# Optimization experiments

Measured on AMD Instinct MI355X. Metric: run time of the kernel, lower is better.

Reference implementation:

```python
import jax, jax.numpy as jnp
import numpy as np

C = 1.0
SQC = C ** 0.5
EPS = 1e-15

def _artanh(x):
    return jnp.arctanh(jnp.clip(x, -1 + 1e-5, 1 - 1e-5))

def _norm(x):
    return jnp.sqrt(jnp.maximum(jnp.sum(x * x, -1, keepdims=True), EPS))

def expmap0(u):
    un = _norm(u)
    return jnp.tanh(SQC * un) * u / (SQC * un)

def logmap0(x):
    xn = _norm(x)
    return _artanh(SQC * xn) * x / (SQC * xn)

def project(x):
    maxnorm = (1.0 - 1e-3) / SQC
    xn = _norm(x)
    return jnp.where(xn > maxnorm, x / xn * maxnorm, x)

def mobius_add(x, y):
    x2 = jnp.sum(x * x, -1, keepdims=True)
    y2 = jnp.sum(y * y, -1, keepdims=True)
    xy = jnp.sum(x * y, -1, keepdims=True)
    num = (1 + 2 * C * xy + C * y2) * x + (1 - C * x2) * y
    den = 1 + 2 * C * xy + C * C * x2 * y2
    return num / jnp.maximum(den, EPS)

def mobius_matvec(M, x):
    xn = _norm(x)
    Mx = x @ M.T
    Mxn = _norm(Mx)
    res = jnp.tanh(Mxn / xn * _artanh(SQC * xn)) * Mx / (Mxn * SQC)
    return jnp.where(Mxn <= 1e-7, jnp.zeros_like(res), res)

def mobius_pointwise_mul(w, x):
    xn = _norm(x)
    wx = w * x
    wxn = _norm(wx)
    res = jnp.tanh(wxn / xn * _artanh(SQC * xn)) * wx / (wxn * SQC)
    return jnp.where(wxn <= 1e-7, jnp.zeros_like(res), res)

def mobius_scalar_mul(r, x):
    # r: [B,1] scalars, x: [P] point -> [B,P]
    xn = _norm(x)
    return jnp.tanh(r * _artanh(SQC * xn)) * x / (xn * SQC)

def poincare_dist(x, y):
    return 2.0 / SQC * _artanh(SQC * _norm(mobius_add(-x, y)))

def dist2plane(x, p, a):
    # x: [B,P], p,a: [K,P] -> [B,K]
    diff = mobius_add(-p[None, :, :], x[:, None, :])  # [B,K,P]
    diff2 = jnp.sum(diff * diff, -1)
    sc_da = jnp.sum(diff * a[None, :, :], -1)
    a_norm = jnp.sqrt(jnp.maximum(jnp.sum(a * a, -1), EPS))  # [K]
    num = 2 * SQC * sc_da
    den = jnp.maximum((1 - C * diff2) * a_norm[None, :], EPS)
    return jnp.arcsinh(num / den) / SQC

def one_rnn_transform(W, h, U, x, b):
    Wh = mobius_matvec(W, h)
    Ux = mobius_matvec(U, x)
    return mobius_add(mobius_add(Wh, Ux), b)

def mobius_gru(x_seq, w_ih, w_hh, b, h0):
    # x_seq: [S,B,E]; w_ih: [3,H,E]; w_hh: [3,H,H]; b: [3,H]
    W_ir, W_ih_, W_iz = w_ih[0], w_ih[1], w_ih[2]
    W_hr, W_hh_, W_hz = w_hh[0], w_hh[1], w_hh[2]
    b_r, b_h, b_z = b[0], b[1], b[2]

    def cell(h, x):
        z = jax.nn.sigmoid(logmap0(one_rnn_transform(W_hz, h, W_iz, x, b_z)))
        r = jax.nn.sigmoid(logmap0(one_rnn_transform(W_hr, h, W_ir, x, b_r)))
        rh = mobius_pointwise_mul(r, h)
        h_tilde = one_rnn_transform(W_hh_, rh, W_ih_, x, b_h)
        delta = mobius_add(-h, h_tilde)
        h_new = mobius_add(h, mobius_pointwise_mul(z, delta))
        return h_new, None

    h_final, _ = jax.lax.scan(cell, h0, x_seq)
    return h_final

def mobius_linear(x, W, b):
    return project(mobius_add(mobius_matvec(W, x), b))


def setup_inputs() -> dict:
    key = jax.random.key(0)
    ks = jax.random.split(key, 20)
    V, E, H, P, K, B, S = 32000, 256, 512, 256, 2, 512, 100
    inp = {
        "embedding": jax.random.normal(ks[0], (V, E), jnp.float32) * 0.1,
        "w_ih_src": jax.random.normal(ks[1], (3, H, E), jnp.float32) * 0.05,
        "w_hh_src": jax.random.normal(ks[2], (3, H, H), jnp.float32) * 0.05,
        "b_src": jax.random.normal(ks[3], (3, H), jnp.float32) * 0.01,
        "w_ih_tgt": jax.random.normal(ks[4], (3, H, E), jnp.float32) * 0.05,
        "w_hh_tgt": jax.random.normal(ks[5], (3, H, H), jnp.float32) * 0.05,
        "b_tgt": jax.random.normal(ks[6], (3, H), jnp.float32) * 0.01,
        "wp_src": jax.random.normal(ks[7], (P, H), jnp.float32) * 0.05,
        "bp_src": jax.random.normal(ks[8], (P,), jnp.float32) * 0.01,
        "wp_tgt": jax.random.normal(ks[9], (P, H), jnp.float32) * 0.05,
        "bp_tgt": jax.random.normal(ks[10], (P,), jnp.float32) * 0.01,
        "dist_bias": jax.random.normal(ks[11], (P,), jnp.float32) * 0.01,
        "plane_p": jax.random.normal(ks[12], (K, P), jnp.float32) * 0.01,
        "plane_a": jax.random.normal(ks[13], (K, P), jnp.float32) * 0.1,
        "source_tokens": jax.random.randint(ks[14], (B, S), 0, V, jnp.int32),
        "target_tokens": jax.random.randint(ks[15], (B, S), 0, V, jnp.int32),
        "alignment": jax.random.randint(ks[16], (B,), 0, B, jnp.int32),
    }
    return inp


def reference(embedding, w_ih_src, w_hh_src, b_src, w_ih_tgt, w_hh_tgt, b_tgt,
              wp_src, bp_src, wp_tgt, bp_tgt, dist_bias, plane_p, plane_a,
              source_tokens, target_tokens, alignment):
    B, S = source_tokens.shape
    H = w_hh_src.shape[-1]
    # euclidean embeddings lifted to the Poincare ball (embedding_type='eucl', hyp cell)
    src = expmap0(embedding[source_tokens]).transpose(1, 0, 2)  # [S,B,E]
    tgt = expmap0(embedding[target_tokens]).transpose(1, 0, 2)
    h0 = jnp.zeros((B, H), src.dtype)
    h_src = mobius_gru(src, w_ih_src, w_hh_src, b_src, h0)
    h_tgt = mobius_gru(tgt, w_ih_tgt, w_hh_tgt, b_tgt, h0)
    h_tgt = h_tgt[alignment]
    src_proj = mobius_linear(h_src, wp_src, bp_src)
    tgt_proj = mobius_linear(h_tgt, wp_tgt, bp_tgt)
    projected = mobius_add(src_proj, tgt_proj)
    d2 = poincare_dist(h_src, h_tgt) ** 2  # [B,1]
    bias = mobius_scalar_mul(d2, dist_bias)  # [B,P]
    projected = mobius_add(projected, bias)
    logits = dist2plane(projected, plane_p, plane_a)  # [B,K]
    return logits
```

## Files before the change

kernel.cpp:

```cpp
#include <hip/hip_runtime.h>
#include <hip/hip_bf16.h>

#define EPSF 1e-15f

typedef __hip_bfloat16 bf16;
typedef __attribute__((ext_vector_type(8))) short short8;
typedef __attribute__((ext_vector_type(4))) float f32x4;

#define F4E(v,i) ((i)==0?(v).x:((i)==1?(v).y:((i)==2?(v).z:(v).w)))
#define U4E(v,i) ((i)==0?(v).x:((i)==1?(v).y:((i)==2?(v).z:(v).w)))

__device__ __forceinline__ float artanh_c(float x) {
  x = fminf(fmaxf(x, -1.f + 1e-5f), 1.f - 1e-5f);
  return 0.5f * log1pf(2.f * x / (1.f - x));
}
__device__ __forceinline__ float sigmoidf(float x) { return 1.f / (1.f + expf(-x)); }
__device__ __forceinline__ float wave_sum(float x) {
#pragma unroll
  for (int o = 32; o > 0; o >>= 1) x += __shfl_xor(x, o);
  return x;
}
__device__ __forceinline__ float bu2f(ushort u) { return __uint_as_float(((unsigned)u) << 16); }
__device__ __forceinline__ ushort f2bu(float v) {
  bf16 t = __float2bfloat16(v);
  union { bf16 b; ushort u; } c; c.b = t; return c.u;
}
__device__ __forceinline__ void split2(float v, ushort& h, ushort& l) {
  h = f2bu(v); l = f2bu(v - bu2f(h));
}

__global__ __launch_bounds__(256) void k_wconv(
    const float* __restrict__ w_ih_src, const float* __restrict__ w_hh_src,
    const float* __restrict__ w_ih_tgt, const float* __restrict__ w_hh_tgt,
    bf16* __restrict__ W0h, bf16* __restrict__ W1h)
{
  const int idx = blockIdx.x * 256 + threadIdx.x;
  float v;
  if (idx < 1835008) {
    const int g = idx / 917504, p = idx % 917504;
    const float* wih = g ? w_ih_tgt : w_ih_src;
    const float* whh = g ? w_hh_tgt : w_hh_src;
    if (p < 524288) {
      const int unit = p >> 9, r = p & 511, lane = r >> 3, e = r & 7;
      const int ct = unit >> 4, ki = unit & 15;
      const int col = ct*16 + (lane & 15), k = ki*32 + (lane >> 4)*8 + e;
      v = (col < 512) ? whh[524288 + col*512 + k]
                      : whh[(col - 512)*512 + k];
    } else {
      const int q = p - 524288;
      const int unit = q >> 9, r = q & 511, lane = r >> 3, e = r & 7;
      const int ct = unit >> 3, ki = unit & 7;
      const int col = ct*16 + (lane & 15), k = ki*32 + (lane >> 4)*8 + e;
      v = (col < 512)  ? wih[262144 + col*256 + k]
        : (col < 1024) ? wih[(col - 512)*256 + k]
                       : wih[131072 + (col - 1024)*256 + k];
    }
    ((ushort*)W0h)[idx] = f2bu(v);
  } else {
    const int j = idx - 1835008;
    if (j >= 524288) return;
    const int g = j >> 18, p = j & 262143;
    const float* whh = g ? w_hh_tgt : w_hh_src;
    const int unit = p >> 9, r = p & 511, lane = r >> 3, e = r & 7;
    const int ct = unit >> 4, ki = unit & 15;
    const int col = ct*16 + (lane & 15), k = ki*32 + (lane >> 4)*8 + e;
    v = whh[262144 + col*512 + k];
    ((ushort*)W1h)[j] = f2bu(v);
  }
}

__device__ __forceinline__ void gate_row(
    const float h[8], const float whz[8], const float whr[8],
    const float uxz[8], const float uxr[8], const float uxh[8],
    const float bz[8], const float br[8],
    float xn_x, float axn_x,
    float rh[8], float pz[8], float puhx[8],
    float& o_xnrh, float& o_axnrh, float& o_y2u, float& o_sh2)
{
  float r60=0, r61=0, r62=0, r63=0, r64_=0, r65=0;
#pragma unroll
  for (int e = 0; e < 8; e++) {
    r60 += h[e]*h[e];     r61 += whz[e]*whz[e]; r62 += whr[e]*whr[e];
    r63 += uxz[e]*uxz[e]; r64_ += uxr[e]*uxr[e]; r65 += uxh[e]*uxh[e];
  }
  r60 = wave_sum(r60); r61 = wave_sum(r61); r62 = wave_sum(r62);
  r63 = wave_sum(r63); r64_ = wave_sum(r64_); r65 = wave_sum(r65);
  const float sh2 = r60;
  const float xn_h = sqrtf(fmaxf(sh2, EPSF)), axn_h = artanh_c(xn_h);
  const float mz = sqrtf(fmaxf(r61, EPSF)); const float tz = tanhf(mz / xn_h * axn_h);
  const float sz = (mz <= 1e-7f) ? 0.f : tz/mz; const float x2z = (mz <= 1e-7f) ? 0.f : tz*tz;
  const float mr = sqrtf(fmaxf(r62, EPSF)); const float tr_ = tanhf(mr / xn_h * axn_h);
  const float sr = (mr <= 1e-7f) ? 0.f : tr_/mr; const float x2r = (mr <= 1e-7f) ? 0.f : tr_*tr_;
  const float muz = sqrtf(fmaxf(r63, EPSF)); const float tuz = tanhf(muz / xn_x * axn_x);
  const float suz = (muz <= 1e-7f) ? 0.f : tuz/muz; const float y2z = (muz <= 1e-7f) ? 0.f : tuz*tuz;
  const float mur = sqrtf(fmaxf(r64_, EPSF)); const float tur = tanhf(mur / xn_x * axn_x);
  const float sur = (mur <= 1e-7f) ? 0.f : tur/mur; const float y2r = (mur <= 1e-7f) ? 0.f : tur*tur;
  const float muh = sqrtf(fmaxf(r65, EPSF)); const float tuh = tanhf(muh / xn_x * axn_x);
  const float suh = (muh <= 1e-7f) ? 0.f : tuh/muh; const float y2u = (muh <= 1e-7f) ? 0.f : tuh*tuh;

  float dd0 = 0, dd1 = 0;
#pragma unroll
  for (int e = 0; e < 8; e++) {
    dd0 += (sz*whz[e])*(suz*uxz[e]);
    dd1 += (sr*whr[e])*(sur*uxr[e]);
  }
  dd0 = wave_sum(dd0); dd1 = wave_sum(dd1);
  float t1z[8], t1r[8];
  {
    const float iv = 1.f / fmaxf(1.f + 2.f*dd0 + x2z*y2z, EPSF);
    const float c1 = 1.f + 2.f*dd0 + y2z, c2 = 1.f - x2z;
#pragma unroll
    for (int e = 0; e < 8; e++) t1z[e] = (c1*(sz*whz[e]) + c2*(suz*uxz[e])) * iv;
  }
  {
    const float iv = 1.f / fmaxf(1.f + 2.f*dd1 + x2r*y2r, EPSF);
    const float c1 = 1.f + 2.f*dd1 + y2r, c2 = 1.f - x2r;
#pragma unroll
    for (int e = 0; e < 8; e++) t1r[e] = (c1*(sr*whr[e]) + c2*(sur*uxr[e])) * iv;
  }
  float e0=0, e1=0, e2=0, e3=0, e4=0, e5=0;
#pragma unroll
  for (int e = 0; e < 8; e++) {
    e0 += t1z[e]*t1z[e]; e1 += t1z[e]*bz[e]; e2 += bz[e]*bz[e];
    e3 += t1r[e]*t1r[e]; e4 += t1r[e]*br[e]; e5 += br[e]*br[e];
  }
  e0 = wave_sum(e0); e1 = wave_sum(e1); e2 = wave_sum(e2);
  e3 = wave_sum(e3); e4 = wave_sum(e4); e5 = wave_sum(e5);
  float t2z[8], t2r[8];
  {
    const float iv = 1.f / fmaxf(1.f + 2.f*e1 + e0*e2, EPSF);
    const float c1 = 1.f + 2.f*e1 + e2, c2 = 1.f - e0;
#pragma unroll
    for (int e = 0; e < 8; e++) t2z[e] = (c1*t1z[e] + c2*bz[e]) * iv;
  }
  {
    const float iv = 1.f / fmaxf(1.f + 2.f*e4 + e3*e5, EPSF);
    const float c1 = 1.f + 2.f*e4 + e5, c2 = 1.f - e3;
#pragma unroll
    for (int e = 0; e < 8; e++) t2r[e] = (c1*t1r[e] + c2*br[e]) * iv;
  }
  float n0 = 0, n1 = 0;
#pragma unroll
  for (int e = 0; e < 8; e++) { n0 += t2z[e]*t2z[e]; n1 += t2r[e]*t2r[e]; }
  n0 = wave_sum(n0); n1 = wave_sum(n1);
  const float nz = sqrtf(fmaxf(n0, EPSF)); const float fz = artanh_c(nz) / nz;
  const float nr = sqrtf(fmaxf(n1, EPSF)); const float frg = artanh_c(nr) / nr;
  float wx[8];
  float rw = 0;
#pragma unroll
  for (int e = 0; e < 8; e++) {
    pz[e] = sigmoidf(fz * t2z[e]);
    const float rr = sigmoidf(frg * t2r[e]);
    wx[e] = rr * h[e];
    rw += wx[e]*wx[e];
  }
  rw = wave_sum(rw);
  const float wxn = sqrtf(fmaxf(rw, EPSF));
  const float trh = tanhf(wxn / xn_h * axn_h);
  const float srh = (wxn <= 1e-7f) ? 0.f : trh / wxn;
  const float xn_rh = (wxn <= 1e-7f) ? sqrtf(EPSF) : fmaxf(trh, sqrtf(EPSF));
#pragma unroll
  for (int e = 0; e < 8; e++) { rh[e] = srh * wx[e]; puhx[e] = suh * uxh[e]; }
  o_xnrh = xn_rh; o_axnrh = artanh_c(xn_rh); o_y2u = y2u; o_sh2 = sh2;
}

__device__ __forceinline__ void update_row(
    const float mt_[8], const float bh[8],
    const float pz[8], const float puhx[8], const float phv[8],
    float p_xnrh, float p_axnrh, float p_y2u, float p_sh2,
    float hnew[8])
{
  float a0s = 0, a1s = 0;
#pragma unroll
  for (int e = 0; e < 8; e++) { a0s += mt_[e]*mt_[e]; a1s += mt_[e]*puhx[e]; }
  a0s = wave_sum(a0s); a1s = wave_sum(a1s);
  const float m = sqrtf(fmaxf(a0s, EPSF));
  const float tt = tanhf(m / p_xnrh * p_axnrh);
  const float st = (m <= 1e-7f) ? 0.f : tt/m;
  const float x2 = (m <= 1e-7f) ? 0.f : tt*tt;
  float t1[8];
  {
    const float xy = st * a1s;
    const float iv = 1.f / fmaxf(1.f + 2.f*xy + x2*p_y2u, EPSF);
    const float c1 = 1.f + 2.f*xy + p_y2u, c2 = 1.f - x2;
#pragma unroll
    for (int e = 0; e < 8; e++) t1[e] = (c1*(st*mt_[e]) + c2*puhx[e]) * iv;
  }
  float b0s = 0, b1s = 0, b2s = 0;
#pragma unroll
  for (int e = 0; e < 8; e++) { b0s += t1[e]*t1[e]; b1s += t1[e]*bh[e]; b2s += bh[e]*bh[e]; }
  b0s = wave_sum(b0s); b1s = wave_sum(b1s); b2s = wave_sum(b2s);
  float ht[8];
  {
    const float iv = 1.f / fmaxf(1.f + 2.f*b1s + b0s*b2s, EPSF);
    const float c1 = 1.f + 2.f*b1s + b2s, c2 = 1.f - b0s;
#pragma unroll
    for (int e = 0; e < 8; e++) ht[e] = (c1*t1[e] + c2*bh[e]) * iv;
  }
  float c0s = 0, c1s = 0;
#pragma unroll
  for (int e = 0; e < 8; e++) { c0s += ht[e]*ht[e]; c1s += phv[e]*ht[e]; }
  c0s = wave_sum(c0s); c1s = wave_sum(c1s);
  float delta[8];
  {
    const float xy = -c1s;
    const float iv = 1.f / fmaxf(1.f + 2.f*xy + p_sh2*c0s, EPSF);
    const float c1 = 1.f + 2.f*xy + c0s, c2 = 1.f - p_sh2;
#pragma unroll
    for (int e = 0; e < 8; e++) delta[e] = (c1*(-phv[e]) + c2*ht[e]) * iv;
  }
  float d0s = 0, d1s = 0, d2s = 0;
#pragma unroll
  for (int e = 0; e < 8; e++) {
    const float ww = pz[e]*delta[e];
    d0s += delta[e]*delta[e]; d1s += ww*ww; d2s += phv[e]*ww;
  }
  d0s = wave_sum(d0s); d1s = wave_sum(d1s); d2s = wave_sum(d2s);
  const float dn = sqrtf(fmaxf(d0s, EPSF));
  const float axnd = artanh_c(dn);
  const float wxn = sqrtf(fmaxf(d1s, EPSF));
  const float tzd = tanhf(wxn / dn * axnd);
  const float szd = (wxn <= 1e-7f) ? 0.f : tzd/wxn;
  const float y2zd = (wxn <= 1e-7f) ? 0.f : tzd*tzd;
  const float xy = szd * d2s;
  const float iv = 1.f / fmaxf(1.f + 2.f*xy + p_sh2*y2zd, EPSF);
  const float c1 = 1.f + 2.f*xy + y2zd, c2 = 1.f - p_sh2;
#pragma unroll
  for (int e = 0; e < 8; e++) hnew[e] = (c1*phv[e] + c2*(szd*pz[e]*delta[e])) * iv;
}

__global__ __launch_bounds__(512, 1) void k_rnn(
    const float* __restrict__ emb, const int* __restrict__ src_t,
    const int* __restrict__ tgt_t, const float* __restrict__ b_src,
    const float* __restrict__ b_tgt,
    const bf16* __restrict__ W0h_, const bf16* __restrict__ W1h_,
    float* __restrict__ yws, float* __restrict__ htmws,
    float* __restrict__ hbuf)
{
  const int bid = blockIdx.x, tid = threadIdx.x;
  const int w = tid >> 6, lane = tid & 63;
  const int fr = lane & 15, kg = lane >> 4;
  const int xcd = bid & 7, slot = bid >> 3;
  const int g = xcd >> 2;
  const int b16 = (xcd & 3) * 8 + slot;
  const bf16* W0h = W0h_ + (size_t)g * 917504;
  const bf16* W1h = W1h_ + (size_t)g * 262144;
  const int* toks = g ? tgt_t : src_t;
  const float* bb = g ? b_tgt : b_src;
  float* ysl = yws + (size_t)bid * 40960;
  float* hsl = htmws + (size_t)bid * 8192;

  __shared__ char L[65536];
  for (int i = tid; i < 2048; i += 512) ((float4*)L)[i] = make_float4(0.f,0.f,0.f,0.f);

  float p_xnx[2], p_axnx[2];
  float pz_[2][8], puhx_[2][8], phh_[2][8];
  float p_xnrh[2], p_axnrh[2], p_y2u[2], p_sh2[2];

#define XLOAD(RI, TOKIDX)                                                        \
  {                                                                              \
    const int row = w*2 + (RI);                                                  \
    const int tok = toks[(b16*16 + row)*100 + (TOKIDX)];                         \
    const float4 ev = ((const float4*)(emb + (size_t)tok * 256))[lane];          \
    float ss = ev.x*ev.x + ev.y*ev.y + ev.z*ev.z + ev.w*ev.w;                    \
    ss = wave_sum(ss);                                                           \
    const float un = sqrtf(fmaxf(ss, EPSF));                                     \
    const float fac = tanhf(un) / un;                                            \
    const float xnv = sqrtf(fmaxf(fac*fac*ss, EPSF));                            \
    p_xnx[RI] = xnv; p_axnx[RI] = artanh_c(xnv);                                 \
    ushort th[4], tl[4];                                                         \
    split2(fac*ev.x, th[0], tl[0]); split2(fac*ev.y, th[1], tl[1]);              \
    split2(fac*ev.z, th[2], tl[2]); split2(fac*ev.w, th[3], tl[3]);              \
    const unsigned xo = (unsigned)((row*512 + lane*8) ^ ((row & 7) << 4));       \
    *(ushort4*)(L + 32768 + xo) = make_ushort4(th[0],th[1],th[2],th[3]);         \
    *(ushort4*)(L + 40960 + xo) = make_ushort4(tl[0],tl[1],tl[2],tl[3]);         \
  }

  XLOAD(0, 0)
  XLOAD(1, 0)
  __syncthreads();

  for (int s = 0; s < 100; s++) {
    {
      const f32x4 z4 = {0.f,0.f,0.f,0.f};
      f32x4 acc[8];
#pragma unroll
      for (int t = 0; t < 8; t++) acc[t] = z4;
#pragma unroll 2
      for (int ki = 0; ki < 16; ki++) {
        short8 bfr[8];
#pragma unroll
        for (int t = 0; t < 8; t++)
          bfr[t] = *(const short8*)(W0h + (size_t)(((w*8 + t)*16 + ki)*512) + lane*8);
        const unsigned ao = (unsigned)((fr*1024 + ki*64 + kg*16) ^ ((fr & 7) << 4));
        const short8 aHi = *(const short8*)(L + ao);
        const short8 aLo = *(const short8*)(L + 16384 + ao);
#pragma unroll
        for (int t = 0; t < 8; t++) {
          acc[t] = __builtin_amdgcn_mfma_f32_16x16x32_bf16(aHi, bfr[t], acc[t], 0,0,0);
          acc[t] = __builtin_amdgcn_mfma_f32_16x16x32_bf16(aLo, bfr[t], acc[t], 0,0,0);
        }
      }
#pragma unroll
      for (int t = 0; t < 8; t++) {
        const int colb = (w*8 + t)*16 + fr;
#pragma unroll
        for (int r = 0; r < 4; r++)
          ysl[(size_t)(kg*4 + r)*2560 + colb] = acc[t][r];
      }
    }
    {
      const f32x4 z4 = {0.f,0.f,0.f,0.f};
      f32x4 acc[12];
#pragma unroll
      for (int t = 0; t < 12; t++) acc[t] = z4;
      for (int ki = 0; ki < 8; ki++) {
        short8 bfr[12];
#pragma unroll
        for (int t = 0; t < 12; t++)
          bfr[t] = *(const short8*)(W0h + 524288 + (size_t)(((w*12 + t)*8 + ki)*512) + lane*8);
        const unsigned ao = (unsigned)((fr*512 + ki*64 + kg*16) ^ ((fr & 7) << 4));
        const short8 aHi = *(const short8*)(L + 32768 + ao);
        const short8 aLo = *(const short8*)(L + 40960 + ao);
#pragma unroll
        for (int t = 0; t < 12; t++) {
          acc[t] = __builtin_amdgcn_mfma_f32_16x16x32_bf16(aHi, bfr[t], acc[t], 0,0,0);
          acc[t] = __builtin_amdgcn_mfma_f32_16x16x32_bf16(aLo, bfr[t], acc[t], 0,0,0);
        }
      }
#pragma unroll
      for (int t = 0; t < 12; t++) {
        const int colb = 1024 + (w*12 + t)*16 + fr;
#pragma unroll
        for (int r = 0; r < 4; r++)
          ysl[(size_t)(kg*4 + r)*2560 + colb] = acc[t][r];
      }
    }
    __syncthreads();

#define PH2_ROW(RI)                                                              \
    {                                                                            \
      const int row = w*2 + (RI);                                                \
      const float* grow = ysl + row * 2560;                                      \
      float h[8], whz[8], whr[8], uxz[8], uxr[8], uxh[8], bz[8], br[8];          \
      _Pragma("unroll")                                                          \
      for (int q = 0; q < 2; q++) {                                              \
        const int j4 = lane + 64*q;                                              \
        const unsigned ho = (unsigned)((row*1024 + j4*8) ^ ((row & 7) << 4));    \
        const ushort4 hh4 = *(const ushort4*)(L + ho);                           \
        const ushort4 hl4 = *(const ushort4*)(L + 16384 + ho);                   \
        const float4 vz  = ((const float4*)grow)[j4];                            \
        const float4 vr  = ((const float4*)(grow + 512))[j4];                    \
        const float4 uz  = ((const float4*)(grow + 1024))[j4];                   \
        const float4 ur  = ((const float4*)(grow + 1536))[j4];                   \
        const float4 uh  = ((const float4*)(grow + 2048))[j4];                   \
        const float4 vbz = ((const float4*)(bb + 1024))[j4];                     \
        const float4 vbr = ((const float4*)bb)[j4];                              \
        _Pragma("unroll")                                                        \
        for (int i = 0; i < 4; i++) {                                            \
          const int e = q*4 + i;                                                 \
          h[e] = bu2f(U4E(hh4,i)) + bu2f(U4E(hl4,i));                            \
          whz[e] = F4E(vz,i); whr[e] = F4E(vr,i);                                \
          uxz[e] = F4E(uz,i); uxr[e] = F4E(ur,i); uxh[e] = F4E(uh,i);            \
          bz[e] = F4E(vbz,i); br[e] = F4E(vbr,i);                               \
        }                                                                        \
      }                                                                          \
      float rh[8];                                                               \
      gate_row(h, whz, whr, uxz, uxr, uxh, bz, br, p_xnx[RI], p_axnx[RI],        \
               rh, pz_[RI], puhx_[RI],                                           \
               p_xnrh[RI], p_axnrh[RI], p_y2u[RI], p_sh2[RI]);                   \
      _Pragma("unroll")                                                          \
      for (int e = 0; e < 8; e++) phh_[RI][e] = h[e];                            \
      _Pragma("unroll")                                                          \
      for (int q = 0; q < 2; q++) {                                              \
        const int j4 = lane + 64*q;                                              \
        const unsigned ro = (unsigned)((row*1024 + j4*8) ^ ((row & 7) << 4));    \
        ushort th[4], tl[4];                                                     \
        _Pragma("unroll")                                                        \
        for (int i = 0; i < 4; i++) split2(rh[q*4+i], th[i], tl[i]);             \
        *(ushort4*)(L + 32768 + ro) = make_ushort4(th[0],th[1],th[2],th[3]);     \
        *(ushort4*)(L + 49152 + ro) = make_ushort4(tl[0],tl[1],tl[2],tl[3]);     \
      }                                                                          \
    }

    PH2_ROW(0)
    PH2_ROW(1)
    __syncthreads();

    {
      const f32x4 z4 = {0.f,0.f,0.f,0.f};
      f32x4 acc[4];
#pragma unroll
      for (int t = 0; t < 4; t++) acc[t] = z4;
#pragma unroll 2
      for (int ki = 0; ki < 16; ki++) {
        short8 bfr[4];
#pragma unroll
        for (int t = 0; t < 4; t++)
          bfr[t] = *(const short8*)(W1h + (size_t)(((w*4 + t)*16 + ki)*512) + lane*8);
        const unsigned ao = (unsigned)((fr*1024 + ki*64 + kg*16) ^ ((fr & 7) << 4));
        const short8 aHi = *(const short8*)(L + 32768 + ao);
        const short8 aLo = *(const short8*)(L + 49152 + ao);
#pragma unroll
        for (int t = 0; t < 4; t++) {
          acc[t] = __builtin_amdgcn_mfma_f32_16x16x32_bf16(aHi, bfr[t], acc[t], 0,0,0);
          acc[t] = __builtin_amdgcn_mfma_f32_16x16x32_bf16(aLo, bfr[t], acc[t], 0,0,0);
        }
      }
#pragma unroll
      for (int t = 0; t < 4; t++) {
        const int colb = (w*4 + t)*16 + fr;
#pragma unroll
        for (int r = 0; r < 4; r++)
          hsl[(size_t)(kg*4 + r)*512 + colb] = acc[t][r];
      }
    }
    __syncthreads();

#define PH4_ROW(RI)                                                              \
    {                                                                            \
      const int row = w*2 + (RI);                                                \
      float mt_[8], bh[8];                                                       \
      _Pragma("unroll")                                                          \
      for (int q = 0; q < 2; q++) {                                              \
        const int j4 = lane + 64*q;                                              \
        const float4 vm = ((const float4*)(hsl + row*512))[j4];                  \
        const float4 vb = ((const float4*)(bb + 512))[j4];                       \
        _Pragma("unroll")                                                        \
        for (int i = 0; i < 4; i++) {                                            \
          mt_[q*4+i] = F4E(vm,i); bh[q*4+i] = F4E(vb,i);                         \
        }                                                                        \
      }                                                                          \
      float hnew[8];                                                             \
      update_row(mt_, bh, pz_[RI], puhx_[RI], phh_[RI],                          \
                 p_xnrh[RI], p_axnrh[RI], p_y2u[RI], p_sh2[RI], hnew);           \
      _Pragma("unroll")                                                          \
      for (int q = 0; q < 2; q++) {                                              \
        const int j4 = lane + 64*q;                                              \
        const unsigned ho = (unsigned)((row*1024 + j4*8) ^ ((row & 7) << 4));    \
        ushort th[4], tl[4];                                                     \
        _Pragma("unroll")                                                        \
        for (int i = 0; i < 4; i++) split2(hnew[q*4+i], th[i], tl[i]);           \
        *(ushort4*)(L + ho) = make_ushort4(th[0],th[1],th[2],th[3]);             \
        *(ushort4*)(L + 16384 + ho) = make_ushort4(tl[0],tl[1],tl[2],tl[3]);     \
        if (s == 99)                                                             \
          ((float4*)(hbuf + (size_t)(g*512 + b16*16 + row)*512))[j4] =           \
              make_float4(hnew[q*4], hnew[q*4+1], hnew[q*4+2], hnew[q*4+3]);     \
      }                                                                          \
      if (s + 1 < 100) XLOAD(RI, s + 1)                                          \
    }

    PH4_ROW(0)
    PH4_ROW(1)
    __syncthreads();
  }
}

__global__ __launch_bounds__(256) void gemm_k(
    const float* __restrict__ hbuf,
    const float* __restrict__ wp_src, const float* __restrict__ wp_tgt,
    const int* __restrict__ alignment,
    float* __restrict__ out)
{
  const int rt = blockIdx.x, ct = blockIdx.y;
  const int rowBase = rt * 64;
  const int tid = threadIdx.x;
  const int chunk = ct >> 2;
  const int colBase = ct * 64, ldo = 512, kdim = 512;
  const float* W = (chunk ? wp_tgt : wp_src) + (size_t)((ct & 3) * 64) * 512;
  const int ar = tid >> 2, ak = (tid & 3) * 4;
  int arow = rowBase + ar;
  if (chunk) arow = 512 + alignment[arow];
  const float* Arow = hbuf + (size_t)arow * kdim;
  const float* Wrow = W + (size_t)(tid >> 2) * kdim + (tid & 3) * 4;

  __shared__ __align__(16) float As[16][68];
  __shared__ __align__(16) float Bs[16][68];
  float acc[4][4] = {{0.f}};
  const int ty = tid >> 4, tx = tid & 15;

  for (int k0 = 0; k0 < kdim; k0 += 16) {
    const float4 av = *(const float4*)(Arow + k0 + ak);
    const float4 bv = *(const float4*)(Wrow + k0);
    const int bj = tid >> 2;
    As[ak + 0][ar] = av.x; As[ak + 1][ar] = av.y; As[ak + 2][ar] = av.z; As[ak + 3][ar] = av.w;
    Bs[ak + 0][bj] = bv.x; Bs[ak + 1][bj] = bv.y; Bs[ak + 2][bj] = bv.z; Bs[ak + 3][bj] = bv.w;
    __syncthreads();
#pragma unroll
    for (int kk = 0; kk < 16; kk++) {
      const float4 a4 = *(const float4*)(&As[kk][ty * 4]);
      const float4 b4 = *(const float4*)(&Bs[kk][tx * 4]);
      acc[0][0] += a4.x * b4.x; acc[0][1] += a4.x * b4.y; acc[0][2] += a4.x * b4.z; acc[0][3] += a4.x * b4.w;
      acc[1][0] += a4.y * b4.x; acc[1][1] += a4.y * b4.y; acc[1][2] += a4.y * b4.z; acc[1][3] += a4.y * b4.w;
      acc[2][0] += a4.z * b4.x; acc[2][1] += a4.z * b4.y; acc[2][2] += a4.z * b4.z; acc[2][3] += a4.z * b4.w;
      acc[3][0] += a4.w * b4.x; acc[3][1] += a4.w * b4.y; acc[3][2] += a4.w * b4.z; acc[3][3] += a4.w * b4.w;
    }
    __syncthreads();
  }
#pragma unroll
  for (int r = 0; r < 4; r++) {
    float4 o; o.x = acc[r][0]; o.y = acc[r][1]; o.z = acc[r][2]; o.w = acc[r][3];
    *(float4*)(out + (size_t)(rowBase + ty * 4 + r) * ldo + colBase + tx * 4) = o;
  }
}

template<int N>
__device__ __forceinline__ void block_reduce(float* v) {
  __shared__ float s[4][N];
  __syncthreads();
  const int lane = threadIdx.x & 63;
  const int wv = threadIdx.x >> 6;
#pragma unroll
  for (int n = 0; n < N; n++) {
    float x = v[n];
#pragma unroll
    for (int o = 32; o > 0; o >>= 1) x += __shfl_down(x, o);
    if (lane == 0) s[wv][n] = x;
  }
  __syncthreads();
#pragma unroll
  for (int n = 0; n < N; n++) v[n] = s[0][n] + s[1][n] + s[2][n] + s[3][n];
}

__global__ __launch_bounds__(256) void k_head(
    const float* __restrict__ hb, const float* __restrict__ mxb,
    const float* __restrict__ bp_src, const float* __restrict__ bp_tgt,
    const float* __restrict__ dist_bias, const float* __restrict__ plane_p,
    const float* __restrict__ plane_a, const int* __restrict__ alignment,
    float* __restrict__ outp)
{
  const int b = blockIdx.x;
  const int t = threadIdx.x;
  const int arow = 512 + alignment[b];
  float hs[2], htg[2];
  hs[0] = hb[(size_t)b * 512 + t];      hs[1] = hb[(size_t)b * 512 + 256 + t];
  htg[0] = hb[(size_t)arow * 512 + t];  htg[1] = hb[(size_t)arow * 512 + 256 + t];
  const float mxs = mxb[(size_t)b * 512 + t];
  const float mxt = mxb[(size_t)b * 512 + 256 + t];
  const float bps = bp_src[t], bpt = bp_tgt[t], db = dist_bias[t];
  const float pp0 = plane_p[t], pp1 = plane_p[256 + t];
  const float pa0 = plane_a[t], pa1 = plane_a[256 + t];

  float rA[5] = {0, 0, 0, 0, 0};
#pragma unroll
  for (int e = 0; e < 2; e++) {
    rA[0] += hs[e] * hs[e]; rA[1] += htg[e] * htg[e]; rA[2] += hs[e] * htg[e];
  }
  rA[3] = mxs * mxs; rA[4] = mxt * mxt;
  block_reduce<5>(rA);
  const float shs = rA[0], sht = rA[1], dot_st = rA[2];
  const float xns = sqrtf(fmaxf(shs, EPSF)), axns = artanh_c(xns);
  const float xnt = sqrtf(fmaxf(sht, EPSF)), axnt = artanh_c(xnt);
  const float ms = sqrtf(fmaxf(rA[3], EPSF)); const float ts = tanhf(ms / xns * axns);
  const float ss = (ms <= 1e-7f) ? 0.f : ts / ms; const float x2s = (ms <= 1e-7f) ? 0.f : ts * ts;
  const float mt = sqrtf(fmaxf(rA[4], EPSF)); const float tt = tanhf(mt / xnt * axnt);
  const float st = (mt <= 1e-7f) ? 0.f : tt / mt; const float x2t = (mt <= 1e-7f) ? 0.f : tt * tt;
  const float vs = ss * mxs, vt = st * mxt;

  float rB[5] = {bps * bps, vs * bps, bpt * bpt, vt * bpt, db * db};
  block_reduce<5>(rB);
  float ps, pt;
  {
    const float y2 = rB[0], xy = rB[1];
    const float iv = 1.f / fmaxf(1.f + 2.f * xy + x2s * y2, EPSF);
    ps = ((1.f + 2.f * xy + y2) * vs + (1.f - x2s) * bps) * iv;
  }
  {
    const float y2 = rB[2], xy = rB[3];
    const float iv = 1.f / fmaxf(1.f + 2.f * xy + x2t * y2, EPSF);
    pt = ((1.f + 2.f * xy + y2) * vt + (1.f - x2t) * bpt) * iv;
  }
  float rC[2] = {ps * ps, pt * pt};
  block_reduce<2>(rC);
  {
    const float n = sqrtf(fmaxf(rC[0], EPSF));
    if (n > 0.999f) ps *= 0.999f / n;
  }
  {
    const float n = sqrtf(fmaxf(rC[1], EPSF));
    if (n > 0.999f) pt *= 0.999f / n;
  }
  float df[2];
  {
    const float xy = -dot_st;
    const float iv = 1.f / fmaxf(1.f + 2.f * xy + shs * sht, EPSF);
    const float c1 = 1.f + 2.f * xy + sht, c2 = 1.f - shs;
#pragma unroll
    for (int e = 0; e < 2; e++) df[e] = (c1 * (-hs[e]) + c2 * htg[e]) * iv;
  }
  float rD[4] = {ps * ps, pt * pt, ps * pt, df[0] * df[0] + df[1] * df[1]};
  block_reduce<4>(rD);
  float pr;
  {
    const float x2 = rD[0], y2 = rD[1], xy = rD[2];
    const float iv = 1.f / fmaxf(1.f + 2.f * xy + x2 * y2, EPSF);
    pr = ((1.f + 2.f * xy + y2) * ps + (1.f - x2) * pt) * iv;
  }
  const float dn = sqrtf(fmaxf(rD[3], EPSF));
  const float dist = 2.f * artanh_c(dn);
  const float d2v = dist * dist;
  const float dbn = sqrtf(fmaxf(rB[4], EPSF));
  const float biasv = tanhf(d2v * artanh_c(dbn)) * db / dbn;

  float rE[3] = {pr * pr, biasv * biasv, pr * biasv};
  block_reduce<3>(rE);
  float pr2;
  {
    const float x2 = rE[0], y2 = rE[1], xy = rE[2];
    const float iv = 1.f / fmaxf(1.f + 2.f * xy + x2 * y2, EPSF);
    pr2 = ((1.f + 2.f * xy + y2) * pr + (1.f - x2) * biasv) * iv;
  }
  float rF[5] = {pp0 * pp0, pp0 * pr2, pp1 * pp1, pp1 * pr2, pr2 * pr2};
  block_reduce<5>(rF);
  float d0, d1;
  {
    const float x2 = rF[0], xy = -rF[1], y2 = rF[4];
    const float iv = 1.f / fmaxf(1.f + 2.f * xy + x2 * y2, EPSF);
    d0 = ((1.f + 2.f * xy + y2) * (-pp0) + (1.f - x2) * pr2) * iv;
  }
  {
    const float x2 = rF[2], xy = -rF[3], y2 = rF[4];
    const float iv = 1.f / fmaxf(1.f + 2.f * xy + x2 * y2, EPSF);
    d1 = ((1.f + 2.f * xy + y2) * (-pp1) + (1.f - x2) * pr2) * iv;
  }
  float rG[6] = {d0 * d0, d0 * pa0, pa0 * pa0, d1 * d1, d1 * pa1, pa1 * pa1};
  block_reduce<6>(rG);
  if (t == 0) {
    const float an0 = sqrtf(fmaxf(rG[2], EPSF));
    const float an1 = sqrtf(fmaxf(rG[5], EPSF));
    outp[b * 2 + 0] = asinhf(2.f * rG[1] / fmaxf((1.f - rG[0]) * an0, EPSF));
    outp[b * 2 + 1] = asinhf(2.f * rG[4] / fmaxf((1.f - rG[3]) * an1, EPSF));
  }
}

extern "C" void kernel_launch(void* const* d_in, const int* in_sizes, int n_in,
                              void* d_out, int out_size, void* d_ws, size_t ws_size,
                              hipStream_t stream) {
  const float* emb       = (const float*)d_in[0];
  const float* w_ih_src  = (const float*)d_in[1];
  const float* w_hh_src  = (const float*)d_in[2];
  const float* b_src     = (const float*)d_in[3];
  const float* w_ih_tgt  = (const float*)d_in[4];
  const float* w_hh_tgt  = (const float*)d_in[5];
  const float* b_tgt     = (const float*)d_in[6];
  const float* wp_src    = (const float*)d_in[7];
  const float* bp_src    = (const float*)d_in[8];
  const float* wp_tgt    = (const float*)d_in[9];
  const float* bp_tgt    = (const float*)d_in[10];
  const float* dist_bias = (const float*)d_in[11];
  const float* plane_p   = (const float*)d_in[12];
  const float* plane_a   = (const float*)d_in[13];
  const int* src_t       = (const int*)d_in[14];
  const int* tgt_t       = (const int*)d_in[15];
  const int* alignment   = (const int*)d_in[16];
  float* outp            = (float*)d_out;

  char* wsb = (char*)d_ws;
  float* yws   = (float*)(wsb + 0);
  float* htmws = (float*)(wsb + 10485760);
  float* hbuf  = (float*)(wsb + 12582912);
  float* mxb   = (float*)(wsb + 14680064);
  bf16*  W0h   = (bf16*)(wsb + 15728640);
  bf16*  W1h   = (bf16*)(wsb + 19398656);

  k_wconv<<<9216, 256, 0, stream>>>(w_ih_src, w_hh_src, w_ih_tgt, w_hh_tgt,
                                    W0h, W1h);
  k_rnn<<<64, 512, 0, stream>>>(emb, src_t, tgt_t, b_src, b_tgt,
                                W0h, W1h, yws, htmws, hbuf);
  gemm_k<<<dim3(8, 8), 256, 0, stream>>>(hbuf, wp_src, wp_tgt, alignment, mxb);
  k_head<<<512, 256, 0, stream>>>(hbuf, mxb, bp_src, bp_tgt, dist_bias,
                                  plane_p, plane_a, alignment, outp);
}
```

Before: 8.191 ms.

## Split RNN batch across 128 blocks of 8 rows, store gates as bf16

The recurrent kernel now launches 128 blocks of 256 threads, each owning 8 batch rows instead of 16, so each wave computes twice as many output columns per MFMA pass. Only half of each 16-row MFMA tile is used, since rows 8-15 repeat rows 0-7. The gate pre-activation scratch is stored as bf16 in global memory, and the hidden-transform scratch moves from global memory into LDS. This spreads the serial 100-step recurrence over more CUs and halves scratch traffic. The cost is wasted MFMA work on the padded rows, twice the total weight streaming across blocks, and reduced precision in the stored gate values.

```diff
diff --git a/kernel.cpp b/kernel.cpp
--- a/kernel.cpp
+++ b/kernel.cpp
@@ -229,29 +229,28 @@
   for (int e = 0; e < 8; e++) hnew[e] = (c1*phv[e] + c2*(szd*pz[e]*delta[e])) * iv;
 }
 
-__global__ __launch_bounds__(512, 1) void k_rnn(
+__global__ __launch_bounds__(256, 1) void k_rnn(
     const float* __restrict__ emb, const int* __restrict__ src_t,
     const int* __restrict__ tgt_t, const float* __restrict__ b_src,
     const float* __restrict__ b_tgt,
     const bf16* __restrict__ W0h_, const bf16* __restrict__ W1h_,
-    float* __restrict__ yws, float* __restrict__ htmws,
-    float* __restrict__ hbuf)
+    ushort* __restrict__ yws, float* __restrict__ hbuf)
 {
   const int bid = blockIdx.x, tid = threadIdx.x;
   const int w = tid >> 6, lane = tid & 63;
   const int fr = lane & 15, kg = lane >> 4;
-  const int xcd = bid & 7, slot = bid >> 3;
-  const int g = xcd >> 2;
-  const int b16 = (xcd & 3) * 8 + slot;
+  const int fr7 = fr & 7;
+  const int g = (bid & 7) >> 2;
+  const int b8 = (bid & 3) * 16 + (bid >> 3);
   const bf16* W0h = W0h_ + (size_t)g * 917504;
   const bf16* W1h = W1h_ + (size_t)g * 262144;
   const int* toks = g ? tgt_t : src_t;
   const float* bb = g ? b_tgt : b_src;
-  float* ysl = yws + (size_t)bid * 40960;
-  float* hsl = htmws + (size_t)bid * 8192;
-
-  __shared__ char L[65536];
-  for (int i = tid; i < 2048; i += 512) ((float4*)L)[i] = make_float4(0.f,0.f,0.f,0.f);
+  ushort* yg = yws + (size_t)bid * 20480;
+
+  __shared__ char L[57600];
+  float* htmL = (float*)(L + 40960);
+  for (int i = tid; i < 1024; i += 256) ((float4*)L)[i] = make_float4(0.f,0.f,0.f,0.f);
 
   float p_xnx[2], p_axnx[2];
   float pz_[2][8], puhx_[2][8], phh_[2][8];
@@ -260,7 +259,7 @@
 #define XLOAD(RI, TOKIDX)                                                        \
   {                                                                              \
     const int row = w*2 + (RI);                                                  \
-    const int tok = toks[(b16*16 + row)*100 + (TOKIDX)];                         \
+    const int tok = toks[(b8*8 + row)*100 + (TOKIDX)];                           \
     const float4 ev = ((const float4*)(emb + (size_t)tok * 256))[lane];          \
     float ss = ev.x*ev.x + ev.y*ev.y + ev.z*ev.z + ev.w*ev.w;                    \
     ss = wave_sum(ss);                                                           \
@@ -272,8 +271,8 @@
     split2(fac*ev.x, th[0], tl[0]); split2(fac*ev.y, th[1], tl[1]);              \
     split2(fac*ev.z, th[2], tl[2]); split2(fac*ev.w, th[3], tl[3]);              \
     const unsigned xo = (unsigned)((row*512 + lane*8) ^ ((row & 7) << 4));       \
-    *(ushort4*)(L + 32768 + xo) = make_ushort4(th[0],th[1],th[2],th[3]);         \
-    *(ushort4*)(L + 40960 + xo) = make_ushort4(tl[0],tl[1],tl[2],tl[3]);         \
+    *(ushort4*)(L + 16384 + xo) = make_ushort4(th[0],th[1],th[2],th[3]);         \
+    *(ushort4*)(L + 20480 + xo) = make_ushort4(tl[0],tl[1],tl[2],tl[3]);         \
   }
 
   XLOAD(0, 0)
@@ -283,33 +282,35 @@
   for (int s = 0; s < 100; s++) {
     {
       const f32x4 z4 = {0.f,0.f,0.f,0.f};
-      f32x4 acc[8];
-#pragma unroll
-      for (int t = 0; t < 8; t++) acc[t] = z4;
-#pragma unroll 2
+      f32x4 acc[16];
+#pragma unroll
+      for (int t = 0; t < 16; t++) acc[t] = z4;
       for (int ki = 0; ki < 16; ki++) {
-        short8 bfr[8];
-#pragma unroll
-        for (int t = 0; t < 8; t++)
-          bfr[t] = *(const short8*)(W0h + (size_t)(((w*8 + t)*16 + ki)*512) + lane*8);
-        const unsigned ao = (unsigned)((fr*1024 + ki*64 + kg*16) ^ ((fr & 7) << 4));
+        short8 bfr[16];
+#pragma unroll
+        for (int t = 0; t < 16; t++)
+          bfr[t] = *(const short8*)(W0h + (size_t)(((w*16 + t)*16 + ki)*512) + lane*8);
+        const unsigned ao = (unsigned)((fr7*1024 + ki*64 + kg*16) ^ (fr7 << 4));
         const short8 aHi = *(const short8*)(L + ao);
-        const short8 aLo = *(const short8*)(L + 16384 + ao);
-#pragma unroll
-        for (int t = 0; t < 8; t++) {
+        const short8 aLo = *(const short8*)(L + 8192 + ao);
+#pragma unroll
+        for (int t = 0; t < 16; t++) {
           acc[t] = __builtin_amdgcn_mfma_f32_16x16x32_bf16(aHi, bfr[t], acc[t], 0,0,0);
           acc[t] = __builtin_amdgcn_mfma_f32_16x16x32_bf16(aLo, bfr[t], acc[t], 0,0,0);
         }
       }
-#pragma unroll
-      for (int t = 0; t < 8; t++) {
-        const int colb = (w*8 + t)*16 + fr;
-#pragma unroll
-        for (int r = 0; r < 4; r++)
-          ysl[(size_t)(kg*4 + r)*2560 + colb] = acc[t][r];
+      if (kg < 2) {
+#pragma unroll
+        for (int t = 0; t < 16; t++) {
+          const int colb = (w*16 + t)*16 + fr;
+#pragma unroll
+          for (int r = 0; r < 4; r++)
+            yg[(size_t)(kg*4 + r)*2560 + colb] = f2bu(acc[t][r]);
+        }
       }
     }
-    {
+#pragma unroll
+    for (int p = 0; p < 2; p++) {
       const f32x4 z4 = {0.f,0.f,0.f,0.f};
       f32x4 acc[12];
 #pragma unroll
@@ -318,22 +319,25 @@
         short8 bfr[12];
 #pragma unroll
         for (int t = 0; t < 12; t++)
-          bfr[t] = *(const short8*)(W0h + 524288 + (size_t)(((w*12 + t)*8 + ki)*512) + lane*8);
-        const unsigned ao = (unsigned)((fr*512 + ki*64 + kg*16) ^ ((fr & 7) << 4));
-        const short8 aHi = *(const short8*)(L + 32768 + ao);
-        const short8 aLo = *(const short8*)(L + 40960 + ao);
+          bfr[t] = *(const short8*)(W0h + 524288 +
+                      (size_t)(((w*24 + p*12 + t)*8 + ki)*512) + lane*8);
+        const unsigned ao = (unsigned)((fr7*512 + ki*64 + kg*16) ^ (fr7 << 4));
+        const short8 aHi = *(const short8*)(L + 16384 + ao);
+        const short8 aLo = *(const short8*)(L + 20480 + ao);
 #pragma unroll
         for (int t = 0; t < 12; t++) {
           acc[t] = __builtin_amdgcn_mfma_f32_16x16x32_bf16(aHi, bfr[t], acc[t], 0,0,0);
           acc[t] = __builtin_amdgcn_mfma_f32_16x16x32_bf16(aLo, bfr[t], acc[t], 0,0,0);
         }
       }
-#pragma unroll
-      for (int t = 0; t < 12; t++) {
-        const int colb = 1024 + (w*12 + t)*16 + fr;
-#pragma unroll
-        for (int r = 0; r < 4; r++)
-          ysl[(size_t)(kg*4 + r)*2560 + colb] = acc[t][r];
+      if (kg < 2) {
+#pragma unroll
+        for (int t = 0; t < 12; t++) {
+          const int colb = 1024 + (w*24 + p*12 + t)*16 + fr;
+#pragma unroll
+          for (int r = 0; r < 4; r++)
+            yg[(size_t)(kg*4 + r)*2560 + colb] = f2bu(acc[t][r]);
+        }
       }
     }
     __syncthreads();
@@ -341,27 +345,28 @@
 #define PH2_ROW(RI)                                                              \
     {                                                                            \
       const int row = w*2 + (RI);                                                \
-      const float* grow = ysl + row * 2560;                                      \
+      const ushort* growu = yg + (size_t)row * 2560;                             \
       float h[8], whz[8], whr[8], uxz[8], uxr[8], uxh[8], bz[8], br[8];          \
       _Pragma("unroll")                                                          \
       for (int q = 0; q < 2; q++) {                                              \
         const int j4 = lane + 64*q;                                              \
         const unsigned ho = (unsigned)((row*1024 + j4*8) ^ ((row & 7) << 4));    \
         const ushort4 hh4 = *(const ushort4*)(L + ho);                           \
-        const ushort4 hl4 = *(const ushort4*)(L + 16384 + ho);                   \
-        const float4 vz  = ((const float4*)grow)[j4];                            \
-        const float4 vr  = ((const float4*)(grow + 512))[j4];                    \
-        const float4 uz  = ((const float4*)(grow + 1024))[j4];                   \
-        const float4 ur  = ((const float4*)(grow + 1536))[j4];                   \
-        const float4 uh  = ((const float4*)(grow + 2048))[j4];                   \
+        const ushort4 hl4 = *(const ushort4*)(L + 8192 + ho);                    \
+        const ushort4 vz  = ((const ushort4*)growu)[j4];                         \
+        const ushort4 vr  = ((const ushort4*)(growu + 512))[j4];                 \
+        const ushort4 uz  = ((const ushort4*)(growu + 1024))[j4];                \
+        const ushort4 ur  = ((const ushort4*)(growu + 1536))[j4];                \
+        const ushort4 uh  = ((const ushort4*)(growu + 2048))[j4];                \
         const float4 vbz = ((const float4*)(bb + 1024))[j4];                     \
         const float4 vbr = ((const float4*)bb)[j4];                              \
         _Pragma("unroll")                                                        \
         for (int i = 0; i < 4; i++) {                                            \
           const int e = q*4 + i;                                                 \
           h[e] = bu2f(U4E(hh4,i)) + bu2f(U4E(hl4,i));                            \
-          whz[e] = F4E(vz,i); whr[e] = F4E(vr,i);                                \
-          uxz[e] = F4E(uz,i); uxr[e] = F4E(ur,i); uxh[e] = F4E(uh,i);            \
+          whz[e] = bu2f(U4E(vz,i)); whr[e] = bu2f(U4E(vr,i));                    \
+          uxz[e] = bu2f(U4E(uz,i)); uxr[e] = bu2f(U4E(ur,i));                    \
+          uxh[e] = bu2f(U4E(uh,i));                                              \
           bz[e] = F4E(vbz,i); br[e] = F4E(vbr,i);                               \
         }                                                                        \
       }                                                                          \
@@ -378,8 +383,8 @@
         ushort th[4], tl[4];                                                     \
         _Pragma("unroll")                                                        \
         for (int i = 0; i < 4; i++) split2(rh[q*4+i], th[i], tl[i]);             \
-        *(ushort4*)(L + 32768 + ro) = make_ushort4(th[0],th[1],th[2],th[3]);     \
-        *(ushort4*)(L + 49152 + ro) = make_ushort4(tl[0],tl[1],tl[2],tl[3]);     \
+        *(ushort4*)(L + 24576 + ro) = make_ushort4(th[0],th[1],th[2],th[3]);     \
+        *(ushort4*)(L + 32768 + ro) = make_ushort4(tl[0],tl[1],tl[2],tl[3]);     \
       }                                                                          \
     }
 
@@ -389,30 +394,31 @@
 
     {
       const f32x4 z4 = {0.f,0.f,0.f,0.f};
-      f32x4 acc[4];
-#pragma unroll
-      for (int t = 0; t < 4; t++) acc[t] = z4;
-#pragma unroll 2
+      f32x4 acc[8];
+#pragma unroll
+      for (int t = 0; t < 8; t++) acc[t] = z4;
       for (int ki = 0; ki < 16; ki++) {
-        short8 bfr[4];
-#pragma unroll
-        for (int t = 0; t < 4; t++)
-          bfr[t] = *(const short8*)(W1h + (size_t)(((w*4 + t)*16 + ki)*512) + lane*8);
-        const unsigned ao = (unsigned)((fr*1024 + ki*64 + kg*16) ^ ((fr & 7) << 4));
-        const short8 aHi = *(const short8*)(L + 32768 + ao);
-        const short8 aLo = *(const short8*)(L + 49152 + ao);
-#pragma unroll
-        for (int t = 0; t < 4; t++) {
+        short8 bfr[8];
+#pragma unroll
+        for (int t = 0; t < 8; t++)
+          bfr[t] = *(const short8*)(W1h + (size_t)(((w*8 + t)*16 + ki)*512) + lane*8);
+        const unsigned ao = (unsigned)((fr7*1024 + ki*64 + kg*16) ^ (fr7 << 4));
+        const short8 aHi = *(const short8*)(L + 24576 + ao);
+        const short8 aLo = *(const short8*)(L + 32768 + ao);
+#pragma unroll
+        for (int t = 0; t < 8; t++) {
           acc[t] = __builtin_amdgcn_mfma_f32_16x16x32_bf16(aHi, bfr[t], acc[t], 0,0,0);
           acc[t] = __builtin_amdgcn_mfma_f32_16x16x32_bf16(aLo, bfr[t], acc[t], 0,0,0);
         }
       }
-#pragma unroll
-      for (int t = 0; t < 4; t++) {
-        const int colb = (w*4 + t)*16 + fr;
-#pragma unroll
-        for (int r = 0; r < 4; r++)
-          hsl[(size_t)(kg*4 + r)*512 + colb] = acc[t][r];
+      if (kg < 2) {
+#pragma unroll
+        for (int t = 0; t < 8; t++) {
+          const int colb = (w*8 + t)*16 + fr;
+#pragma unroll
+          for (int r = 0; r < 4; r++)
+            htmL[(kg*4 + r)*520 + colb] = acc[t][r];
+        }
       }
     }
     __syncthreads();
@@ -424,7 +430,7 @@
       _Pragma("unroll")                                                          \
       for (int q = 0; q < 2; q++) {                                              \
         const int j4 = lane + 64*q;                                              \
-        const float4 vm = ((const float4*)(hsl + row*512))[j4];                  \
+        const float4 vm = ((const float4*)(htmL + row*520))[j4];                 \
         const float4 vb = ((const float4*)(bb + 512))[j4];                       \
         _Pragma("unroll")                                                        \
         for (int i = 0; i < 4; i++) {                                            \
@@ -442,9 +448,9 @@
         _Pragma("unroll")                                                        \
         for (int i = 0; i < 4; i++) split2(hnew[q*4+i], th[i], tl[i]);           \
         *(ushort4*)(L + ho) = make_ushort4(th[0],th[1],th[2],th[3]);             \
-        *(ushort4*)(L + 16384 + ho) = make_ushort4(tl[0],tl[1],tl[2],tl[3]);     \
+        *(ushort4*)(L + 8192 + ho) = make_ushort4(tl[0],tl[1],tl[2],tl[3]);      \
         if (s == 99)                                                             \
-          ((float4*)(hbuf + (size_t)(g*512 + b16*16 + row)*512))[j4] =           \
+          ((float4*)(hbuf + (size_t)(g*512 + b8*8 + row)*512))[j4] =             \
               make_float4(hnew[q*4], hnew[q*4+1], hnew[q*4+2], hnew[q*4+3]);     \
       }                                                                          \
       if (s + 1 < 100) XLOAD(RI, s + 1)                                          \
@@ -656,17 +662,16 @@
   float* outp            = (float*)d_out;
 
   char* wsb = (char*)d_ws;
-  float* yws   = (float*)(wsb + 0);
-  float* htmws = (float*)(wsb + 10485760);
-  float* hbuf  = (float*)(wsb + 12582912);
-  float* mxb   = (float*)(wsb + 14680064);
-  bf16*  W0h   = (bf16*)(wsb + 15728640);
-  bf16*  W1h   = (bf16*)(wsb + 19398656);
+  ushort* yws  = (ushort*)(wsb + 0);
+  float* hbuf  = (float*)(wsb + 5242880);
+  float* mxb   = (float*)(wsb + 7340032);
+  bf16*  W0h   = (bf16*)(wsb + 8388608);
+  bf16*  W1h   = (bf16*)(wsb + 12058624);
 
   k_wconv<<<9216, 256, 0, stream>>>(w_ih_src, w_hh_src, w_ih_tgt, w_hh_tgt,
                                     W0h, W1h);
-  k_rnn<<<64, 512, 0, stream>>>(emb, src_t, tgt_t, b_src, b_tgt,
-                                W0h, W1h, yws, htmws, hbuf);
+  k_rnn<<<128, 256, 0, stream>>>(emb, src_t, tgt_t, b_src, b_tgt,
+                                 W0h, W1h, yws, hbuf);
   gemm_k<<<dim3(8, 8), 256, 0, stream>>>(hbuf, wp_src, wp_tgt, alignment, mxb);
   k_head<<<512, 256, 0, stream>>>(hbuf, mxb, bp_src, bp_tgt, dist_bias,
                                   plane_p, plane_a, alignment, outp);
```

Measured after the change: 9.828 ms. +20.0%, slower.

## Keep GRU gate pre-activations in LDS as bf16 instead of global workspace

Applied to the files above, without the earlier changes.

The per-step gate GEMM outputs (16 rows x 2560 cols) are now written as bf16 into a swizzled region of enlarged dynamic shared memory (144KB) rather than as fp32 to a per-block global workspace slice. The pointwise phase reads them back from LDS. This removes a global write/read round trip on the sequential critical path of each of the 100 timesteps. In exchange the gate pre-activations lose precision to bf16, and LDS usage rises sharply. The unroll-2 pragmas on the MFMA k-loops are also dropped.

```diff
diff --git a/kernel.cpp b/kernel.cpp
--- a/kernel.cpp
+++ b/kernel.cpp
@@ -229,14 +229,15 @@
   for (int e = 0; e < 8; e++) hnew[e] = (c1*phv[e] + c2*(szd*pz[e]*delta[e])) * iv;
 }
 
+#define YADDR(row, byteoff) (65536u + ((unsigned)((row)*5120 + (byteoff)) ^ (((row)&7)<<4)))
 __global__ __launch_bounds__(512, 1) void k_rnn(
     const float* __restrict__ emb, const int* __restrict__ src_t,
     const int* __restrict__ tgt_t, const float* __restrict__ b_src,
     const float* __restrict__ b_tgt,
     const bf16* __restrict__ W0h_, const bf16* __restrict__ W1h_,
-    float* __restrict__ yws, float* __restrict__ htmws,
-    float* __restrict__ hbuf)
+    float* __restrict__ htmws, float* __restrict__ hbuf)
 {
+  extern __shared__ char L[];
   const int bid = blockIdx.x, tid = threadIdx.x;
   const int w = tid >> 6, lane = tid & 63;
   const int fr = lane & 15, kg = lane >> 4;
@@ -247,10 +248,8 @@
   const bf16* W1h = W1h_ + (size_t)g * 262144;
   const int* toks = g ? tgt_t : src_t;
   const float* bb = g ? b_tgt : b_src;
-  float* ysl = yws + (size_t)bid * 40960;
   float* hsl = htmws + (size_t)bid * 8192;
 
-  __shared__ char L[65536];
   for (int i = tid; i < 2048; i += 512) ((float4*)L)[i] = make_float4(0.f,0.f,0.f,0.f);
 
   float p_xnx[2], p_axnx[2];
@@ -286,7 +285,6 @@
       f32x4 acc[8];
 #pragma unroll
       for (int t = 0; t < 8; t++) acc[t] = z4;
-#pragma unroll 2
       for (int ki = 0; ki < 16; ki++) {
         short8 bfr[8];
 #pragma unroll
@@ -305,8 +303,10 @@
       for (int t = 0; t < 8; t++) {
         const int colb = (w*8 + t)*16 + fr;
 #pragma unroll
-        for (int r = 0; r < 4; r++)
-          ysl[(size_t)(kg*4 + r)*2560 + colb] = acc[t][r];
+        for (int r = 0; r < 4; r++) {
+          const int row = kg*4 + r;
+          *(ushort*)(L + YADDR(row, colb*2)) = f2bu(acc[t][r]);
+        }
       }
     }
     {
@@ -332,8 +332,10 @@
       for (int t = 0; t < 12; t++) {
         const int colb = 1024 + (w*12 + t)*16 + fr;
 #pragma unroll
-        for (int r = 0; r < 4; r++)
-          ysl[(size_t)(kg*4 + r)*2560 + colb] = acc[t][r];
+        for (int r = 0; r < 4; r++) {
+          const int row = kg*4 + r;
+          *(ushort*)(L + YADDR(row, colb*2)) = f2bu(acc[t][r]);
+        }
       }
     }
     __syncthreads();
@@ -341,7 +343,6 @@
 #define PH2_ROW(RI)                                                              \
     {                                                                            \
       const int row = w*2 + (RI);                                                \
-      const float* grow = ysl + row * 2560;                                      \
       float h[8], whz[8], whr[8], uxz[8], uxr[8], uxh[8], bz[8], br[8];          \
       _Pragma("unroll")                                                          \
       for (int q = 0; q < 2; q++) {                                              \
@@ -349,19 +350,20 @@
         const unsigned ho = (unsigned)((row*1024 + j4*8) ^ ((row & 7) << 4));    \
         const ushort4 hh4 = *(const ushort4*)(L + ho);                           \
         const ushort4 hl4 = *(const ushort4*)(L + 16384 + ho);                   \
-        const float4 vz  = ((const float4*)grow)[j4];                            \
-        const float4 vr  = ((const float4*)(grow + 512))[j4];                    \
-        const float4 uz  = ((const float4*)(grow + 1024))[j4];                   \
-        const float4 ur  = ((const float4*)(grow + 1536))[j4];                   \
-        const float4 uh  = ((const float4*)(grow + 2048))[j4];                   \
+        const ushort4 vz  = *(const ushort4*)(L + YADDR(row, j4*8));             \
+        const ushort4 vr  = *(const ushort4*)(L + YADDR(row, 1024 + j4*8));      \
+        const ushort4 uz  = *(const ushort4*)(L + YADDR(row, 2048 + j4*8));      \
+        const ushort4 ur  = *(const ushort4*)(L + YADDR(row, 3072 + j4*8));      \
+        const ushort4 uh  = *(const ushort4*)(L + YADDR(row, 4096 + j4*8));      \
         const float4 vbz = ((const float4*)(bb + 1024))[j4];                     \
         const float4 vbr = ((const float4*)bb)[j4];                              \
         _Pragma("unroll")                                                        \
         for (int i = 0; i < 4; i++) {                                            \
           const int e = q*4 + i;                                                 \
           h[e] = bu2f(U4E(hh4,i)) + bu2f(U4E(hl4,i));                            \
-          whz[e] = F4E(vz,i); whr[e] = F4E(vr,i);                                \
-          uxz[e] = F4E(uz,i); uxr[e] = F4E(ur,i); uxh[e] = F4E(uh,i);            \
+          whz[e] = bu2f(U4E(vz,i)); whr[e] = bu2f(U4E(vr,i));                    \
+          uxz[e] = bu2f(U4E(uz,i)); uxr[e] = bu2f(U4E(ur,i));                    \
+          uxh[e] = bu2f(U4E(uh,i));                                              \
           bz[e] = F4E(vbz,i); br[e] = F4E(vbr,i);                               \
         }                                                                        \
       }                                                                          \
@@ -392,7 +394,6 @@
       f32x4 acc[4];
 #pragma unroll
       for (int t = 0; t < 4; t++) acc[t] = z4;
-#pragma unroll 2
       for (int ki = 0; ki < 16; ki++) {
         short8 bfr[4];
 #pragma unroll
@@ -656,17 +657,19 @@
   float* outp            = (float*)d_out;
 
   char* wsb = (char*)d_ws;
-  float* yws   = (float*)(wsb + 0);
-  float* htmws = (float*)(wsb + 10485760);
-  float* hbuf  = (float*)(wsb + 12582912);
-  float* mxb   = (float*)(wsb + 14680064);
-  bf16*  W0h   = (bf16*)(wsb + 15728640);
-  bf16*  W1h   = (bf16*)(wsb + 19398656);
+  float* htmws = (float*)(wsb + 0);
+  float* hbuf  = (float*)(wsb + 2097152);
+  float* mxb   = (float*)(wsb + 4194304);
+  bf16*  W0h   = (bf16*)(wsb + 5242880);
+  bf16*  W1h   = (bf16*)(wsb + 8912896);
+
+  hipFuncSetAttribute(reinterpret_cast<const void*>(k_rnn),
+                      hipFuncAttributeMaxDynamicSharedMemorySize, 147456);
 
   k_wconv<<<9216, 256, 0, stream>>>(w_ih_src, w_hh_src, w_ih_tgt, w_hh_tgt,
                                     W0h, W1h);
-  k_rnn<<<64, 512, 0, stream>>>(emb, src_t, tgt_t, b_src, b_tgt,
-                                W0h, W1h, yws, htmws, hbuf);
+  k_rnn<<<64, 512, 147456, stream>>>(emb, src_t, tgt_t, b_src, b_tgt,
+                                     W0h, W1h, htmws, hbuf);
   gemm_k<<<dim3(8, 8), 256, 0, stream>>>(hbuf, wp_src, wp_tgt, alignment, mxb);
   k_head<<<512, 256, 0, stream>>>(hbuf, mxb, bp_src, bp_tgt, dist_bias,
                                   plane_p, plane_a, alignment, outp);
```

New measurement: 11.58 ms. +41.4%, slower.
